# Performance work log

Hardware: AMD Instinct MI355X
Metric: run time of the kernel (lower is better)

## Reference

```python
import jax, jax.numpy as jnp
import numpy as np

B, S, D, H = 4, 4096, 1024, 1024


def log_g(x):
    # where(x >= 0, log(relu(x) + 0.5), -softplus(-x)); relu(x)+0.5 >= 0.5 so log is safe
    return jnp.where(x >= 0, jnp.log(jax.nn.relu(x) + 0.5), -jax.nn.softplus(-x))


def setup_inputs() -> dict:
    key = jax.random.key(0)
    ks = jax.random.split(key, 8)
    scale = 1.0 / np.sqrt(D)
    return {
        "x_t": jax.random.normal(ks[0], (B, S, D), dtype=jnp.float32),
        "pre_h": jax.random.normal(ks[1], (B, 1, H), dtype=jnp.float32),
        "W_f": jax.random.uniform(ks[2], (H, D), jnp.float32, -scale, scale),
        "b_f": jax.random.uniform(ks[3], (H,), jnp.float32, -scale, scale),
        "W_i": jax.random.uniform(ks[4], (H, D), jnp.float32, -scale, scale),
        "b_i": jax.random.uniform(ks[5], (H,), jnp.float32, -scale, scale),
        "W_h": jax.random.uniform(ks[6], (H, D), jnp.float32, -scale, scale),
        "b_h": jax.random.uniform(ks[7], (H,), jnp.float32, -scale, scale),
    }


def reference(x_t, pre_h, W_f, b_f, W_i, b_i, W_h, b_h):
    sp = jax.nn.softplus
    f_pre = jnp.einsum("bsd,hd->bsh", x_t, W_f) + b_f
    i_pre = jnp.einsum("bsd,hd->bsh", x_t, W_i) + b_i
    h_pre = jnp.einsum("bsd,hd->bsh", x_t, W_h) + b_h

    diff = sp(-f_pre) - sp(-i_pre)
    log_f = -sp(diff)        # (B, S, H)
    log_i = -sp(-diff)       # (B, S, H)

    log_h0 = log_g(pre_h)                 # (B, 1, H)
    log_tilde_h = log_g(h_pre)            # (B, S, H)
    log_values = jnp.concatenate([log_h0, log_i + log_tilde_h], axis=1)  # (B, S+1, H)

    # parallel_scan_log: pad cumsum at END of seq dim (as in source: F.pad(..., (0,0,0,1)))
    a_star = jnp.pad(jnp.cumsum(log_f, axis=1), ((0, 0), (0, 1), (0, 0)))  # (B, S+1, H)
    log_h0_plus_b_star = jax.lax.cumlogsumexp(log_values - a_star, axis=1)
    log_h = a_star + log_h0_plus_b_star
    return jnp.exp(log_h)[:, 1:]  # (B, S, H)
```

## Files before the change

### kernel.cpp

```cpp
#include <hip/hip_runtime.h>
#include <hip/hip_bf16.h>
#include <math.h>

#define B_DIM 4
#define S_DIM 4096
#define K_DIM 1024
#define H_DIM 1024
#define M_DIM (B_DIM * S_DIM)

#define BMT 128
#define BNT 64
#define KT_ITERS (K_DIM / 32)

#define NCHUNK 64
#define CLEN (S_DIM / NCHUNK)

typedef __attribute__((ext_vector_type(8))) _Float16 f16x8;
typedef __attribute__((ext_vector_type(4))) _Float16 f16x4;
typedef __attribute__((ext_vector_type(4))) float f32x4;

__device__ __forceinline__ float sp_f(float x) {
    return fmaxf(x, 0.0f) + __logf(1.0f + __expf(-fabsf(x)));
}
__device__ __forceinline__ float log_g_f(float x) {
    return (x >= 0.0f) ? __logf(x + 0.5f) : -sp_f(-x);
}
__device__ __forceinline__ float logaddexp_f(float a, float b) {
    float m = fmaxf(a, b);
    return m + __logf(1.0f + __expf(-fabsf(a - b)));
}
__device__ __forceinline__ float exp_sat(float x) {
    return __expf(fminf(x, 85.0f));
}

__device__ __forceinline__ void gl_lds16(const void* g, void* l) {
    __builtin_amdgcn_global_load_lds(
        (const __attribute__((address_space(1))) unsigned int*)g,
        (__attribute__((address_space(3))) unsigned int*)l, 16, 0, 0);
}

__global__ __launch_bounds__(256) void conv_f16(
    const float* __restrict__ src, _Float16* __restrict__ dst, int n4)
{
    int i = blockIdx.x * 256 + threadIdx.x;
    if (i >= n4) return;
    float4 v = ((const float4*)src)[i];
    f16x4 o = {(_Float16)v.x, (_Float16)v.y, (_Float16)v.z, (_Float16)v.w};
    ((f16x4*)dst)[i] = o;
}

__global__ __launch_bounds__(256, 3) void gemm3(
    const _Float16* __restrict__ xh,
    const _Float16* __restrict__ wh,
    const float* __restrict__ bfp, const float* __restrict__ bip,
    const float* __restrict__ bhp,
    _Float16* __restrict__ lf_out, _Float16* __restrict__ w_out)
{
    __shared__ __align__(16) char smem[20480];

    const int tid = threadIdx.x;
    const int lane = tid & 63;
    const int wv = tid >> 6;
    const int wm = wv >> 1;
    const int wn = wv & 1;

    const int row0 = blockIdx.y * BMT;
    const int col0 = blockIdx.x * BNT;

    const int arow = tid & 127, akq = tid >> 7;
    unsigned ga0 = (unsigned)(((row0 + arow) * K_DIM + akq * 8) * 2);
    const int brow = tid & 63, bkq = tid >> 6;
    unsigned gb0 = (unsigned)(((0 * H_DIM + col0 + brow) * K_DIM + bkq * 8) * 2);
    unsigned gb1 = (unsigned)(((1 * H_DIM + col0 + brow) * K_DIM + bkq * 8) * 2);
    unsigned gb2 = (unsigned)(((2 * H_DIM + col0 + brow) * K_DIM + bkq * 8) * 2);

    const char* __restrict__ px = (const char*)xh;
    const char* __restrict__ pw = (const char*)wh;

    int aoff[4], boff[2];
#pragma unroll
    for (int mi = 0; mi < 4; ++mi)
        aoff[mi] = ((lane >> 4) << 11) + ((wm * 64 + mi * 16 + (lane & 15)) << 4);
#pragma unroll
    for (int nj = 0; nj < 2; ++nj)
        boff[nj] = ((lane >> 4) << 10) + ((wn * 32 + nj * 16 + (lane & 15)) << 4);

    f32x4 acc[3][4][2];
#pragma unroll
    for (int g = 0; g < 3; ++g)
#pragma unroll
        for (int mi = 0; mi < 4; ++mi)
#pragma unroll
            for (int nj = 0; nj < 2; ++nj)
                acc[g][mi][nj] = (f32x4){0.f, 0.f, 0.f, 0.f};

    for (int kt = 0; kt < KT_ITERS; ++kt) {
        __syncthreads();
        gl_lds16(px + ga0, smem + tid * 16);
        gl_lds16(px + ga0 + 32, smem + 4096 + tid * 16);
        gl_lds16(pw + gb0, smem + 8192 + tid * 16);
        gl_lds16(pw + gb1, smem + 12288 + tid * 16);
        gl_lds16(pw + gb2, smem + 16384 + tid * 16);
        ga0 += 64; gb0 += 64; gb1 += 64; gb2 += 64;
        __syncthreads();

        f16x8 a[4];
#pragma unroll
        for (int mi = 0; mi < 4; ++mi)
            a[mi] = *(const f16x8*)(smem + aoff[mi]);
#pragma unroll
        for (int g = 0; g < 3; ++g) {
            const char* bb = smem + 8192 + g * 4096;
            f16x8 b0 = *(const f16x8*)(bb + boff[0]);
            f16x8 b1 = *(const f16x8*)(bb + boff[1]);
#pragma unroll
            for (int mi = 0; mi < 4; ++mi) {
                acc[g][mi][0] = __builtin_amdgcn_mfma_f32_16x16x32_f16(a[mi], b0, acc[g][mi][0], 0, 0, 0);
                acc[g][mi][1] = __builtin_amdgcn_mfma_f32_16x16x32_f16(a[mi], b1, acc[g][mi][1], 0, 0, 0);
            }
        }
    }

    int nidx[2];
    float bfv[2], biv[2], bhv[2];
#pragma unroll
    for (int nj = 0; nj < 2; ++nj) {
        nidx[nj] = col0 + wn * 32 + nj * 16 + (lane & 15);
        bfv[nj] = bfp[nidx[nj]];
        biv[nj] = bip[nidx[nj]];
        bhv[nj] = bhp[nidx[nj]];
    }
#pragma unroll
    for (int mi = 0; mi < 4; ++mi) {
#pragma unroll
        for (int r = 0; r < 4; ++r) {
            int m = row0 + wm * 64 + mi * 16 + ((lane >> 4) << 2) + r;
#pragma unroll
            for (int nj = 0; nj < 2; ++nj) {
                float f_pre = acc[0][mi][nj][r] + bfv[nj];
                float i_pre = acc[1][mi][nj][r] + biv[nj];
                float h_pre = acc[2][mi][nj][r] + bhv[nj];
                float diff = sp_f(-f_pre) - sp_f(-i_pre);
                float lfv = -sp_f(diff);
                float wv_ = -sp_f(-diff) + log_g_f(h_pre);
                size_t o = (size_t)m * H_DIM + nidx[nj];
                lf_out[o] = (_Float16)lfv;
                w_out[o] = (_Float16)wv_;
            }
        }
    }
}

__global__ __launch_bounds__(256) void scan_pass_a(
    const _Float16* __restrict__ lf, const _Float16* __restrict__ w,
    float2* __restrict__ agg)
{
    int tid = blockIdx.x * blockDim.x + threadIdx.x;
    int h = tid & (H_DIM - 1);
    int b = (tid >> 10) & (B_DIM - 1);
    int q = tid >> 12;

    int tstart = q * CLEN + 1;
    int tend = (q == NCHUNK - 1) ? (S_DIM - 1) : (q * CLEN + CLEN);

    size_t idx = (size_t)(b * S_DIM + tstart) * H_DIM + h;
    float c = 0.0f, r = -INFINITY;
    for (int t = tstart; t <= tend; ++t) {
        c += (float)lf[idx];
        r = logaddexp_f(r, (float)w[idx - H_DIM] - c);
        idx += H_DIM;
    }
    agg[(size_t)(b * H_DIM + h) * NCHUNK + q] = make_float2(c, r);
}

__global__ __launch_bounds__(256) void scan_pass_b(
    const _Float16* __restrict__ lf, const float* __restrict__ preh,
    const float2* __restrict__ agg, float2* __restrict__ prefix)
{
    int col = blockIdx.x * blockDim.x + threadIdx.x;
    int h = col & (H_DIM - 1);
    int b = col >> 10;

    float lf0 = (float)lf[(size_t)(b * S_DIM) * H_DIM + h];
    float C = lf0;
    float R = log_g_f(preh[b * H_DIM + h]) - lf0;
    for (int q = 0; q < NCHUNK; ++q) {
        prefix[(size_t)col * NCHUNK + q] = make_float2(C, R);
        float2 a = agg[(size_t)col * NCHUNK + q];
        float Rn = logaddexp_f(R, a.y - C);
        C += a.x;
        R = Rn;
    }
}

__global__ __launch_bounds__(256) void scan_pass_c(
    const _Float16* __restrict__ lf, const _Float16* __restrict__ w,
    const float2* __restrict__ prefix, float* __restrict__ out)
{
    int tid = blockIdx.x * blockDim.x + threadIdx.x;
    int h = tid & (H_DIM - 1);
    int b = (tid >> 10) & (B_DIM - 1);
    int q = tid >> 12;

    float2 p = prefix[(size_t)(b * H_DIM + h) * NCHUNK + q];
    float C = p.x, R = p.y;

    int tstart = q * CLEN + 1;
    int tend = (q == NCHUNK - 1) ? (S_DIM - 1) : (q * CLEN + CLEN);

    size_t idx = (size_t)(b * S_DIM + tstart) * H_DIM + h;
    for (int t = tstart; t <= tend; ++t) {
        C += (float)lf[idx];
        R = logaddexp_f(R, (float)w[idx - H_DIM] - C);
        out[idx - H_DIM] = exp_sat(C + R);
        idx += H_DIM;
    }
    if (q == NCHUNK - 1) {
        R = logaddexp_f(R, (float)w[idx - H_DIM]);
        out[idx - H_DIM] = exp_sat(R);
    }
}

extern "C" void kernel_launch(void* const* d_in, const int* in_sizes, int n_in,
                              void* d_out, int out_size, void* d_ws, size_t ws_size,
                              hipStream_t stream) {
    const float* x    = (const float*)d_in[0];
    const float* preh = (const float*)d_in[1];
    const float* Wf   = (const float*)d_in[2];
    const float* bf   = (const float*)d_in[3];
    const float* Wi   = (const float*)d_in[4];
    const float* bi   = (const float*)d_in[5];
    const float* Wh   = (const float*)d_in[6];
    const float* bh   = (const float*)d_in[7];
    float* out = (float*)d_out;

    _Float16* xh = (_Float16*)d_ws;
    _Float16* wh = xh + (size_t)M_DIM * K_DIM;
    _Float16* lf = wh + (size_t)3 * H_DIM * K_DIM;
    _Float16* wbuf = lf + (size_t)M_DIM * H_DIM;
    float2* agg = (float2*)(wbuf + (size_t)M_DIM * H_DIM);
    float2* prefix = agg + (size_t)B_DIM * H_DIM * NCHUNK;

    conv_f16<<<(M_DIM * K_DIM / 4) / 256, 256, 0, stream>>>(x, xh, M_DIM * K_DIM / 4);
    conv_f16<<<(H_DIM * K_DIM / 4) / 256, 256, 0, stream>>>(Wf, wh, H_DIM * K_DIM / 4);
    conv_f16<<<(H_DIM * K_DIM / 4) / 256, 256, 0, stream>>>(
        Wi, wh + (size_t)H_DIM * K_DIM, H_DIM * K_DIM / 4);
    conv_f16<<<(H_DIM * K_DIM / 4) / 256, 256, 0, stream>>>(
        Wh, wh + (size_t)2 * H_DIM * K_DIM, H_DIM * K_DIM / 4);

    gemm3<<<dim3(H_DIM / BNT, M_DIM / BMT), 256, 0, stream>>>(
        xh, wh, bf, bi, bh, lf, wbuf);

    scan_pass_a<<<(B_DIM * H_DIM * NCHUNK) / 256, 256, 0, stream>>>(lf, wbuf, agg);
    scan_pass_b<<<(B_DIM * H_DIM) / 256, 256, 0, stream>>>(lf, preh, agg, prefix);
    scan_pass_c<<<(B_DIM * H_DIM * NCHUNK) / 256, 256, 0, stream>>>(lf, wbuf, prefix, out);
}
```

Baseline: 392.7 us.

## Double-buffer LDS tiles in fused GEMM K-loop to overlap loads with MFMA

Splits the shared tile into two LDS buffers so the next K-slice is loaded from global memory into one buffer while MFMAs run on the other. This cuts the per-iteration synchronisation from two barriers to one and is meant to hide global-to-LDS load latency behind compute. It also raises wave priority around the MFMA bursts with s_setprio. In exchange, LDS use per block doubles to 40 KB, which could limit how many blocks fit per CU.

```diff
diff --git a/kernel.cpp b/kernel.cpp
--- a/kernel.cpp
+++ b/kernel.cpp
@@ -56,7 +56,8 @@
     const float* __restrict__ bhp,
     _Float16* __restrict__ lf_out, _Float16* __restrict__ w_out)
 {
-    __shared__ __align__(16) char smem[20480];
+    __shared__ __align__(16) char smemA[20480];
+    __shared__ __align__(16) char smemB[20480];
 
     const int tid = threadIdx.x;
     const int lane = tid & 63;
@@ -94,32 +95,53 @@
             for (int nj = 0; nj < 2; ++nj)
                 acc[g][mi][nj] = (f32x4){0.f, 0.f, 0.f, 0.f};
 
-    for (int kt = 0; kt < KT_ITERS; ++kt) {
+#define PREFETCH(nb) do { \
+    gl_lds16(px + ga0,      (nb) + tid * 16); \
+    gl_lds16(px + ga0 + 32, (nb) + 4096 + tid * 16); \
+    gl_lds16(pw + gb0, (nb) + 8192  + tid * 16); \
+    gl_lds16(pw + gb1, (nb) + 12288 + tid * 16); \
+    gl_lds16(pw + gb2, (nb) + 16384 + tid * 16); \
+    ga0 += 64; gb0 += 64; gb1 += 64; gb2 += 64; \
+    __builtin_amdgcn_sched_barrier(0); } while (0)
+
+#define COMPUTE(sb) do { \
+    f16x8 a_[4]; \
+    _Pragma("unroll") \
+    for (int mi = 0; mi < 4; ++mi) \
+        a_[mi] = *(const f16x8*)((sb) + aoff[mi]); \
+    _Pragma("unroll") \
+    for (int g = 0; g < 3; ++g) { \
+        const char* bb_ = (sb) + 8192 + g * 4096; \
+        f16x8 b0_ = *(const f16x8*)(bb_ + boff[0]); \
+        f16x8 b1_ = *(const f16x8*)(bb_ + boff[1]); \
+        __builtin_amdgcn_s_setprio(1); \
+        _Pragma("unroll") \
+        for (int mi = 0; mi < 4; ++mi) { \
+            acc[g][mi][0] = __builtin_amdgcn_mfma_f32_16x16x32_f16(a_[mi], b0_, acc[g][mi][0], 0, 0, 0); \
+            acc[g][mi][1] = __builtin_amdgcn_mfma_f32_16x16x32_f16(a_[mi], b1_, acc[g][mi][1], 0, 0, 0); \
+        } \
+        __builtin_amdgcn_s_setprio(0); \
+    } } while (0)
+
+    PREFETCH(smemA);
+    __syncthreads();
+
+#pragma unroll 1
+    for (int it = 0; it < (KT_ITERS - 2) / 2; ++it) {
+        PREFETCH(smemB);
+        COMPUTE(smemA);
         __syncthreads();
-        gl_lds16(px + ga0, smem + tid * 16);
-        gl_lds16(px + ga0 + 32, smem + 4096 + tid * 16);
-        gl_lds16(pw + gb0, smem + 8192 + tid * 16);
-        gl_lds16(pw + gb1, smem + 12288 + tid * 16);
-        gl_lds16(pw + gb2, smem + 16384 + tid * 16);
-        ga0 += 64; gb0 += 64; gb1 += 64; gb2 += 64;
+        PREFETCH(smemA);
+        COMPUTE(smemB);
         __syncthreads();
-
-        f16x8 a[4];
-#pragma unroll
-        for (int mi = 0; mi < 4; ++mi)
-            a[mi] = *(const f16x8*)(smem + aoff[mi]);
-#pragma unroll
-        for (int g = 0; g < 3; ++g) {
-            const char* bb = smem + 8192 + g * 4096;
-            f16x8 b0 = *(const f16x8*)(bb + boff[0]);
-            f16x8 b1 = *(const f16x8*)(bb + boff[1]);
-#pragma unroll
-            for (int mi = 0; mi < 4; ++mi) {
-                acc[g][mi][0] = __builtin_amdgcn_mfma_f32_16x16x32_f16(a[mi], b0, acc[g][mi][0], 0, 0, 0);
-                acc[g][mi][1] = __builtin_amdgcn_mfma_f32_16x16x32_f16(a[mi], b1, acc[g][mi][1], 0, 0, 0);
-            }
-        }
-    }
+    }
+    PREFETCH(smemB);
+    COMPUTE(smemA);
+    __syncthreads();
+    COMPUTE(smemB);
+
+#undef PREFETCH
+#undef COMPUTE
 
     int nidx[2];
     float bfv[2], biv[2], bhv[2];
```

Measured after the change: 388.6 us. About the same (-1.0%).
